# Kernel tuning notes

Hardware: AMD Instinct MI355X
Metric: run time of the kernel (lower is better)

The kernel has to match this reference:

```python
import jax, jax.numpy as jnp
import numpy as np

N_QUBITS = 4


def _apply_1q(state, U, q):
    """Apply a 2x2 gate U (shape (2,2) or batched (b,2,2)) to qubit q of state (b,2,2,2,2)."""
    s = jnp.moveaxis(state, 1 + q, -1)
    if U.ndim == 3:
        s = jnp.einsum('bij,b...j->b...i', U, s)
    else:
        s = jnp.einsum('ij,b...j->b...i', U, s)
    return jnp.moveaxis(s, -1, 1 + q)


def _apply_cnot(state, c, t):
    """CNOT with control qubit c, target qubit t."""
    s = jnp.moveaxis(state, (1 + c, 1 + t), (-2, -1))
    s = jnp.stack([s[..., 0, :], s[..., 1, ::-1]], axis=-2)  # flip target where control=1
    return jnp.moveaxis(s, (-2, -1), (1 + c, 1 + t))


def _ry_mat(theta):
    """Batched RY matrix, theta (b,) -> (b,2,2) complex64."""
    c = jnp.cos(theta * 0.5).astype(jnp.complex64)
    s = jnp.sin(theta * 0.5).astype(jnp.complex64)
    return jnp.stack([jnp.stack([c, -s], -1), jnp.stack([s, c], -1)], -2)


def _rot_mat(phi, theta, omega):
    """PennyLane Rot(phi, theta, omega) = RZ(omega) RY(theta) RZ(phi), scalar params -> (2,2) complex64."""
    c = jnp.cos(theta * 0.5).astype(jnp.complex64)
    s = jnp.sin(theta * 0.5).astype(jnp.complex64)
    ep = jnp.exp(-0.5j * (phi + omega).astype(jnp.complex64))  # e^{-i(phi+omega)/2}
    em = jnp.exp(0.5j * (phi - omega).astype(jnp.complex64))   # e^{+i(phi-omega)/2}
    row0 = jnp.stack([c * ep, -s * em])
    row1 = jnp.stack([s * jnp.conj(em), c * jnp.conj(ep)])
    return jnp.stack([row0, row1])


def _circuit(x, params):
    b = x.shape[0]
    n_layers = params.shape[0]
    # The 64 sequential RY(x[i]) on wire i%4 commute (same axis) and compose
    # additively: RY(a)RY(b) = RY(a+b). Exact same math, fused.
    angles = x.reshape(b, -1, N_QUBITS).sum(axis=1)  # (b, 4)
    state = jnp.zeros((b,) + (2,) * N_QUBITS, jnp.complex64)
    state = state.at[(slice(None),) + (0,) * N_QUBITS].set(1.0)  # |0000>
    for q in range(N_QUBITS):
        state = _apply_1q(state, _ry_mat(angles[:, q]), q)
    for l in range(n_layers):
        for q in range(N_QUBITS):
            state = _apply_1q(state, _rot_mat(params[l, q, 0], params[l, q, 1], params[l, q, 2]), q)
        for q in range(N_QUBITS - 1):
            state = _apply_cnot(state, q, q + 1)
        state = _apply_cnot(state, N_QUBITS - 1, 0)
    probs = jnp.abs(state) ** 2  # (b,2,2,2,2), real
    z = jnp.array([1.0, -1.0], jnp.float32)
    evs = []
    for q in range(N_QUBITS):
        zq = z.reshape((1,) + (1,) * q + (2,) + (1,) * (N_QUBITS - 1 - q))
        evs.append((probs * zq).sum(axis=tuple(range(1, N_QUBITS + 1))))
    return jnp.stack(evs, axis=-1)  # (b, 4): <Z_0..Z_3>


def setup_inputs() -> dict:
    key = jax.random.key(0)
    k1, k2 = jax.random.split(key)
    x = jax.random.normal(k1, (131072, 64), dtype=jnp.float32)
    params = jax.random.normal(k2, (2, 4, 3), dtype=jnp.float32)
    return {"x": x, "params": params}


def reference(x, params):
    return _circuit(x, params)
```

## Files before the change

kernel.cpp:

```cpp
#include <hip/hip_runtime.h>
#include <hip/hip_bf16.h>


__global__ void qc_setup(const float* __restrict__ params, float4* __restrict__ C4)
{
    __shared__ float  Ur[16][16];
    __shared__ float  Ui[16][16];
    __shared__ float4 Mlds[256];
    const int tid = threadIdx.x;

    if (tid < 16) {
        const int col = tid;
        float ur[16], ui[16];
        #pragma unroll
        for (int k = 0; k < 16; ++k) { ur[k] = (k == col) ? 1.f : 0.f; ui[k] = 0.f; }

        #pragma unroll
        for (int l = 0; l < 2; ++l) {
            #pragma unroll
            for (int q = 0; q < 4; ++q) {
                const float phi = params[l*12 + q*3 + 0];
                const float th  = params[l*12 + q*3 + 1];
                const float om  = params[l*12 + q*3 + 2];
                const float ct = cosf(0.5f*th), st = sinf(0.5f*th);
                const float ap = 0.5f*(phi + om), am = 0.5f*(phi - om);
                const float cap = cosf(ap), sap = sinf(ap);
                const float cam = cosf(am), sam = sinf(am);
                const float u00r =  ct*cap, u00i = -ct*sap;
                const float u01r = -st*cam, u01i = -st*sam;
                const float u10r =  st*cam, u10i = -st*sam;
                const float u11r =  ct*cap, u11i =  ct*sap;
                const int bit = 1 << (3 - q);
                #pragma unroll
                for (int k = 0; k < 16; ++k) {
                    if (k & bit) continue;
                    const int k1 = k | bit;
                    const float arr = ur[k],  aii = ui[k];
                    const float brr = ur[k1], bii = ui[k1];
                    ur[k]  = u00r*arr - u00i*aii + u01r*brr - u01i*bii;
                    ui[k]  = u00r*aii + u00i*arr + u01r*bii + u01i*brr;
                    ur[k1] = u10r*arr - u10i*aii + u11r*brr - u11i*bii;
                    ui[k1] = u10r*aii + u10i*arr + u11r*bii + u11i*brr;
                }
            }
            const int cs[4] = {0,1,2,3}, ts[4] = {1,2,3,0};
            #pragma unroll
            for (int e = 0; e < 4; ++e) {
                const int cb = 3 - cs[e], tb = 3 - ts[e];
                float nr[16], ni[16];
                #pragma unroll
                for (int k = 0; k < 16; ++k) {
                    const int src = ((k >> cb) & 1) ? (k ^ (1 << tb)) : k;
                    nr[k] = ur[src]; ni[k] = ui[src];
                }
                #pragma unroll
                for (int k = 0; k < 16; ++k) { ur[k] = nr[k]; ui[k] = ni[k]; }
            }
        }
        #pragma unroll
        for (int k = 0; k < 16; ++k) { Ur[k][col] = ur[k]; Ui[k][col] = ui[k]; }
    }
    __syncthreads();

    {
        const int i = tid >> 4, j = tid & 15;
        float m0 = 0.f, m1 = 0.f, m2 = 0.f, m3 = 0.f;
        #pragma unroll
        for (int k = 0; k < 16; ++k) {
            const float dot = Ur[k][i]*Ur[k][j] + Ui[k][i]*Ui[k][j];
            m0 += ((k >> 3) & 1) ? -dot : dot;
            m1 += ((k >> 2) & 1) ? -dot : dot;
            m2 += ((k >> 1) & 1) ? -dot : dot;
            m3 += ( k       & 1) ? -dot : dot;
        }
        float4 o; o.x = m0; o.y = m1; o.z = m2; o.w = m3;
        Mlds[tid] = o;
    }
    __syncthreads();

    if (tid < 81) {
        int d[4]; int tt = tid;
        d[0] = tt % 3; tt /= 3; d[1] = tt % 3; tt /= 3; d[2] = tt % 3; d[3] = tt / 3;
        float ax = 0.f, ay = 0.f, az = 0.f, aw = 0.f;
        #pragma unroll
        for (int combo = 0; combo < 16; ++combo) {
            int i = 0, j = 0; float w = 1.f;
            #pragma unroll
            for (int q = 0; q < 4; ++q) {
                const int o = (combo >> q) & 1;
                int bi, bj; float wq;
                if (d[q] == 2)      { bi = o; bj = 1 - o; wq = 0.5f; }
                else if (d[q] == 1) { bi = o; bj = o;     wq = o ? -0.5f : 0.5f; }
                else                { bi = o; bj = o;     wq = 0.5f; }
                i |= bi << (3 - q); j |= bj << (3 - q);
                w *= wq;
            }
            const float4 m = Mlds[i*16 + j];
            ax = fmaf(w, m.x, ax);
            ay = fmaf(w, m.y, ay);
            az = fmaf(w, m.z, az);
            aw = fmaf(w, m.w, aw);
        }
        float4 c; c.x = ax; c.y = ay; c.z = az; c.w = aw;
        C4[tid] = c;
    }
}

__global__ __launch_bounds__(256) void qc_main(const float4* __restrict__ x4,
                                               const float4* __restrict__ C4,
                                               float4* __restrict__ out4)
{
    const int b = blockIdx.x * 256 + threadIdx.x;
    const float4* row = x4 + ((size_t)b << 4);

    float a0 = 0.f, a1 = 0.f, a2 = 0.f, a3 = 0.f;
    #pragma unroll
    for (int j = 0; j < 16; ++j) {
        const float4 v = row[j];
        a0 += v.x; a1 += v.y; a2 += v.z; a3 += v.w;
    }

    float c0,s0,c1,s1,c2,s2,c3,s3;
    __sincosf(a0, &s0, &c0);
    __sincosf(a1, &s1, &c1);
    __sincosf(a2, &s2, &c2);
    __sincosf(a3, &s3, &c3);

    const float g0[3] = {1.f, c0, s0};
    const float g1[3] = {1.f, c1, s1};
    const float g2[3] = {1.f, c2, s2};
    const float g3[3] = {1.f, c3, s3};
    float P01[9], P23[9];
    #pragma unroll
    for (int e1 = 0; e1 < 3; ++e1)
        #pragma unroll
        for (int e0 = 0; e0 < 3; ++e0) {
            P01[e0 + 3*e1] = g0[e0] * g1[e1];
            P23[e0 + 3*e1] = g2[e0] * g3[e1];
        }

    float ax = 0.f, ay = 0.f, az = 0.f, aw = 0.f;
    #pragma unroll
    for (int t = 0; t < 81; ++t) {
        const float T = P01[t % 9] * P23[t / 9];
        const float4 m = C4[t];
        ax = fmaf(T, m.x, ax);
        ay = fmaf(T, m.y, ay);
        az = fmaf(T, m.z, az);
        aw = fmaf(T, m.w, aw);
    }
    float4 r; r.x = ax; r.y = ay; r.z = az; r.w = aw;
    out4[b] = r;
}

extern "C" void kernel_launch(void* const* d_in, const int* in_sizes, int n_in,
                              void* d_out, int out_size, void* d_ws, size_t ws_size,
                              hipStream_t stream)
{
    const float* x      = (const float*)d_in[0];
    const float* params = (const float*)d_in[1];
    float*       out    = (float*)d_out;
    float4*      C4     = (float4*)d_ws;

    qc_setup<<<1, 256, 0, stream>>>(params, C4);

    const int batch = in_sizes[0] / 64;
    qc_main<<<batch / 256, 256, 0, stream>>>(
        (const float4*)x, (const float4*)C4, (float4*)out);
}
```

Before: 84.84 us.

## Fuse coefficient setup into main kernel, recomputing per block in LDS

Merges the single-block setup kernel into the main kernel so every block recomputes the 81 observable coefficients into shared memory instead of reading them from a workspace buffer written by a separate launch. This removes one kernel launch and the serialized single-block dependency. The cost is redundant per-block setup work (16-thread serial gate simulation plus two syncs) and extra shared memory. Precise sincos calls are also replaced with fast intrinsics.

Measured after the change: 79.53 us. -6.3%, faster.

```diff
diff --git a/kernel.cpp b/kernel.cpp
--- a/kernel.cpp
+++ b/kernel.cpp
@@ -2,11 +2,14 @@
 #include <hip/hip_bf16.h>
 
 
-__global__ void qc_setup(const float* __restrict__ params, float4* __restrict__ C4)
+__global__ __launch_bounds__(256) void qc_fused(const float4* __restrict__ x4,
+                                                const float*  __restrict__ params,
+                                                float4*       __restrict__ out4)
 {
     __shared__ float  Ur[16][16];
     __shared__ float  Ui[16][16];
     __shared__ float4 Mlds[256];
+    __shared__ float4 Clds[81];
     const int tid = threadIdx.x;
 
     if (tid < 16) {
@@ -22,10 +25,10 @@
                 const float phi = params[l*12 + q*3 + 0];
                 const float th  = params[l*12 + q*3 + 1];
                 const float om  = params[l*12 + q*3 + 2];
-                const float ct = cosf(0.5f*th), st = sinf(0.5f*th);
-                const float ap = 0.5f*(phi + om), am = 0.5f*(phi - om);
-                const float cap = cosf(ap), sap = sinf(ap);
-                const float cam = cosf(am), sam = sinf(am);
+                float st, ct, sap, cap, sam, cam;
+                __sincosf(0.5f*th,        &st,  &ct);
+                __sincosf(0.5f*(phi+om),  &sap, &cap);
+                __sincosf(0.5f*(phi-om),  &sam, &cam);
                 const float u00r =  ct*cap, u00i = -ct*sap;
                 const float u01r = -st*cam, u01i = -st*sam;
                 const float u10r =  st*cam, u10i = -st*sam;
@@ -102,15 +105,11 @@
             aw = fmaf(w, m.w, aw);
         }
         float4 c; c.x = ax; c.y = ay; c.z = az; c.w = aw;
-        C4[tid] = c;
+        Clds[tid] = c;
     }
-}
+    __syncthreads();
 
-__global__ __launch_bounds__(256) void qc_main(const float4* __restrict__ x4,
-                                               const float4* __restrict__ C4,
-                                               float4* __restrict__ out4)
-{
-    const int b = blockIdx.x * 256 + threadIdx.x;
+    const int b = blockIdx.x * 256 + tid;
     const float4* row = x4 + ((size_t)b << 4);
 
     float a0 = 0.f, a1 = 0.f, a2 = 0.f, a3 = 0.f;
@@ -143,7 +142,7 @@
     #pragma unroll
     for (int t = 0; t < 81; ++t) {
         const float T = P01[t % 9] * P23[t / 9];
-        const float4 m = C4[t];
+        const float4 m = Clds[t];
         ax = fmaf(T, m.x, ax);
         ay = fmaf(T, m.y, ay);
         az = fmaf(T, m.z, az);
@@ -160,11 +159,9 @@
     const float* x      = (const float*)d_in[0];
     const float* params = (const float*)d_in[1];
     float*       out    = (float*)d_out;
-    float4*      C4     = (float4*)d_ws;
-
-    qc_setup<<<1, 256, 0, stream>>>(params, C4);
+    (void)d_ws; (void)ws_size;
 
     const int batch = in_sizes[0] / 64;
-    qc_main<<<batch / 256, 256, 0, stream>>>(
-        (const float4*)x, (const float4*)C4, (float4*)out);
+    qc_fused<<<batch / 256, 256, 0, stream>>>(
+        (const float4*)x, params, (float4*)out);
 }
```
